# Optimization experiments

Measured on AMD Instinct MI355X. Metric: run time of the kernel, lower is better.

## Reference

```python
import jax, jax.numpy as jnp
import numpy as np


def setup_inputs() -> dict:
    key = jax.random.key(0)
    k1, k2 = jax.random.split(key)
    latents = jax.random.normal(k1, (32, 1024, 64), dtype=jnp.float32)
    codebook = jax.random.normal(k2, (8192, 64), dtype=jnp.float32)
    return {"latents": latents, "codebook": codebook}


def reference(latents, codebook):
    # Faithful to: cdist(latents_flat, codebook) -> argmin(dim=1) -> reshape(B, L)
    B, L, D = latents.shape
    x = latents.reshape(-1, D)                         # (N, D)
    x2 = jnp.sum(x * x, axis=1, keepdims=True)         # (N, 1)
    c2 = jnp.sum(codebook * codebook, axis=1)          # (K,)
    # (N, K) distance matrix, then argmin reduction
    d2 = x2 - 2.0 * (x @ codebook.T) + c2[None, :]
    indices = jnp.argmin(d2, axis=1)                   # (N,)
    return indices.reshape(B, L)
```

## Files before the change

kernel.cpp:

```cpp
#include <hip/hip_runtime.h>
#include <stdint.h>


#define N_TOTAL 32768
#define K_CODES 8192
#define EPS_GAP 0.008f

typedef __attribute__((ext_vector_type(4)))  float  floatx4;
typedef __attribute__((ext_vector_type(8)))  __bf16 bf16x8;

#define O_C2    0u
#define O_CBSW  32768u
#define O_PS1   2129920u
#define O_PS2   2654208u
#define O_PI1   3178496u
#define O_CNT   3702784u
#define O_LIST  3703040u
#define O_SLOT  3834112u
#define WS_NEED 4096256u

__device__ __forceinline__ unsigned int fkey(float s) {
    unsigned int u = __float_as_uint(s);
    return (u & 0x80000000u) ? ~u : (u | 0x80000000u);
}

__device__ __forceinline__ void load_lds16(const void* g, void* l) {
    __builtin_amdgcn_global_load_lds(
        (const __attribute__((address_space(1))) unsigned int*)g,
        (__attribute__((address_space(3))) unsigned int*)l, 16, 0, 0);
}

__global__ __launch_bounds__(256) void vq_prep(
    const float4* __restrict__ cb, uint4* __restrict__ cbSw,
    float* __restrict__ c2, int* __restrict__ cnt) {
    __shared__ float red[256];
    const int m = threadIdx.x & 31, g = threadIdx.x >> 5;
    const int rb = blockIdx.x;
    if (rb == 0 && threadIdx.x == 0) *cnt = 0;
    float4 a = cb[(size_t)(rb * 32 + m) * 16 + g * 2];
    float4 b = cb[(size_t)(rb * 32 + m) * 16 + g * 2 + 1];
    float x[8] = {a.x, a.y, a.z, a.w, b.x, b.y, b.z, b.w};
    bf16x8 hv, lv;
    float ss = 0.f;
#pragma unroll
    for (int i = 0; i < 8; ++i) {
        float v  = x[i];
        __bf16 hb = (__bf16)v;
        float r  = v - (float)hb;
        hv[i] = hb;
        lv[i] = (__bf16)r;
        ss += v * v;
    }
    cbSw[(size_t)rb * 512 + g * 32 + m]       = __builtin_bit_cast(uint4, hv);
    cbSw[(size_t)rb * 512 + (8 + g) * 32 + m] = __builtin_bit_cast(uint4, lv);
    red[threadIdx.x] = ss;
    __syncthreads();
    if (threadIdx.x < 32) {
        float s = 0.f;
#pragma unroll
        for (int gg = 0; gg < 8; ++gg) s += red[threadIdx.x + 32 * gg];
        c2[rb * 32 + threadIdx.x] = s;
    }
}

__global__ __launch_bounds__(256, 4) void vq_mfma(
    const float4* __restrict__ lat, const uint4* __restrict__ cbSw,
    const float* __restrict__ c2,
    float* __restrict__ pS1, float* __restrict__ pS2, int* __restrict__ pI1) {
    __shared__ uint4 Bs[2][1024];
    const int tid = threadIdx.x;
    const int wr = tid >> 6, lane = tid & 63;
    const int c16 = lane & 15, h4 = lane >> 4;

    const int q0 = blockIdx.x * 128 + wr * 32 + c16;
    bf16x8 aH[2][2], aL[2][2];
#pragma unroll
    for (int qt = 0; qt < 2; ++qt)
#pragma unroll
    for (int c = 0; c < 2; ++c) {
        float4 v0 = lat[(size_t)(q0 + qt * 16) * 16 + c * 8 + h4 * 2];
        float4 v1 = lat[(size_t)(q0 + qt * 16) * 16 + c * 8 + h4 * 2 + 1];
        float x[8] = {v0.x, v0.y, v0.z, v0.w, v1.x, v1.y, v1.z, v1.w};
#pragma unroll
        for (int j = 0; j < 8; ++j) {
            float v  = x[j];
            __bf16 hb = (__bf16)v;
            aH[qt][c][j] = hb;
            aL[qt][c][j] = (__bf16)(v - (float)hb);
        }
    }

    float t1[2][4], t2[2][4]; int i1[2][4];
#pragma unroll
    for (int qt = 0; qt < 2; ++qt)
#pragma unroll
    for (int r = 0; r < 4; ++r) { t1[qt][r] = -3e38f; t2[qt][r] = -3e38f; i1[qt][r] = 0; }

    const int kBase = blockIdx.y * 2048;
    const uint4* srcBase = cbSw + ((size_t)(kBase >> 5) << 9);
    const float* c2g = c2 + kBase + c16;

    float ccCur[4], ccNxt[4];
#pragma unroll
    for (int T = 0; T < 4; ++T) ccCur[T] = c2g[T * 16];
#pragma unroll
    for (int i = 0; i < 4; ++i)
        load_lds16(&srcBase[wr * 256 + i * 64 + lane], &Bs[0][wr * 256 + i * 64]);
    __syncthreads();

    int cur = 0;
    for (int stage = 0; stage < 32; ++stage) {
        if (stage + 1 < 32) {
            const uint4* sp = srcBase + (size_t)(stage + 1) * 1024;
#pragma unroll
            for (int i = 0; i < 4; ++i)
                load_lds16(&sp[wr * 256 + i * 64 + lane],
                           &Bs[cur ^ 1][wr * 256 + i * 64]);
#pragma unroll
            for (int T = 0; T < 4; ++T)
                ccNxt[T] = c2g[(stage + 1) * 64 + T * 16];
        }

        const int colBase = kBase + stage * 64 + c16;

        __builtin_amdgcn_s_setprio(1);
#pragma unroll
        for (int T = 0; T < 4; ++T) {
            const float nn = -0.5f * ccCur[T];
            const int col = colBase + T * 16;
            const int bb = (T >> 1) * 512 + (T & 1) * 16 + c16 + h4 * 32;
            bf16x8 bH0 = __builtin_bit_cast(bf16x8, Bs[cur][bb]);
            bf16x8 bH1 = __builtin_bit_cast(bf16x8, Bs[cur][bb + 128]);
            bf16x8 bL0 = __builtin_bit_cast(bf16x8, Bs[cur][bb + 256]);
            bf16x8 bL1 = __builtin_bit_cast(bf16x8, Bs[cur][bb + 384]);
#pragma unroll
            for (int qt = 0; qt < 2; ++qt) {
                floatx4 acc = {nn, nn, nn, nn};
                acc = __builtin_amdgcn_mfma_f32_16x16x32_bf16(aH[qt][0], bH0, acc, 0, 0, 0);
                acc = __builtin_amdgcn_mfma_f32_16x16x32_bf16(aH[qt][1], bH1, acc, 0, 0, 0);
                acc = __builtin_amdgcn_mfma_f32_16x16x32_bf16(aL[qt][0], bH0, acc, 0, 0, 0);
                acc = __builtin_amdgcn_mfma_f32_16x16x32_bf16(aL[qt][1], bH1, acc, 0, 0, 0);
                acc = __builtin_amdgcn_mfma_f32_16x16x32_bf16(aH[qt][0], bL0, acc, 0, 0, 0);
                acc = __builtin_amdgcn_mfma_f32_16x16x32_bf16(aH[qt][1], bL1, acc, 0, 0, 0);
#pragma unroll
                for (int r = 0; r < 4; ++r) {
                    float a = acc[r];
                    bool gt = a > t1[qt][r];
                    t2[qt][r] = __builtin_amdgcn_fmed3f(a, t1[qt][r], t2[qt][r]);
                    t1[qt][r] = fmaxf(t1[qt][r], a);
                    i1[qt][r] = gt ? col : i1[qt][r];
                }
            }
        }
        __builtin_amdgcn_s_setprio(0);

        __syncthreads();
#pragma unroll
        for (int T = 0; T < 4; ++T) ccCur[T] = ccNxt[T];
        cur ^= 1;
    }

#pragma unroll
    for (int mask = 1; mask <= 8; mask <<= 1) {
#pragma unroll
        for (int qt = 0; qt < 2; ++qt)
#pragma unroll
        for (int r = 0; r < 4; ++r) {
            float o1 = __shfl_xor(t1[qt][r], mask);
            float o2 = __shfl_xor(t2[qt][r], mask);
            int   oi = __shfl_xor(i1[qt][r], mask);
            float n2 = fmaxf(fmaxf(t2[qt][r], o2), fminf(t1[qt][r], o1));
            bool take = (o1 > t1[qt][r]) || (o1 == t1[qt][r] && oi < i1[qt][r]);
            t1[qt][r] = take ? o1 : t1[qt][r];
            i1[qt][r] = take ? oi : i1[qt][r];
            t2[qt][r] = n2;
        }
    }

    if (c16 == 0) {
        const int o0 = blockIdx.y * N_TOTAL;
#pragma unroll
        for (int qt = 0; qt < 2; ++qt) {
            const int qb = blockIdx.x * 128 + wr * 32 + qt * 16 + h4 * 4;
#pragma unroll
            for (int r = 0; r < 4; ++r) {
                pS1[o0 + qb + r] = -2.f * t1[qt][r];
                pS2[o0 + qb + r] = -2.f * t2[qt][r];
                pI1[o0 + qb + r] = i1[qt][r];
            }
        }
    }
}

__global__ void vq_merge4(const float* __restrict__ pS1, const float* __restrict__ pS2,
                          const int* __restrict__ pI1, int* __restrict__ out,
                          int* __restrict__ cnt, int* __restrict__ list,
                          unsigned long long* __restrict__ slot) {
    int q = blockIdx.x * 256 + threadIdx.x;
    float g1 = 3e38f, g2 = 3e38f;
    int   gi = 0x7FFFFFFF;
#pragma unroll
    for (int p = 0; p < 4; ++p) {
        float s1p = pS1[p * N_TOTAL + q];
        float s2p = pS2[p * N_TOTAL + q];
        int   i1p = pI1[p * N_TOTAL + q];
        bool take = (s1p < g1) || (s1p == g1 && i1p < gi);
        g2 = fminf(g2, fminf(s2p, take ? g1 : s1p));
        if (take) { g1 = s1p; gi = i1p; }
    }
    out[q] = gi;
    if (g2 - g1 < EPS_GAP) {
        int e = atomicAdd(cnt, 1);
        list[e] = q;
        slot[e] = 0xFFFFFFFFFFFFFFFFull;
    }
}

__global__ __launch_bounds__(256) void vq_exact2(
    const float4* __restrict__ lat, const float4* __restrict__ cb,
    const float* __restrict__ c2, const int* __restrict__ cnt,
    const int* __restrict__ list, unsigned long long* __restrict__ slot) {
    __shared__ float qv[4][64];
    const int n = *cnt;
    const int totalChunks = n * 8;
    const int wInB = threadIdx.x >> 6;
    const int lane = threadIdx.x & 63;

    for (int base = blockIdx.x * 4; base < totalChunks; base += gridDim.x * 4) {
        const int c = base + wInB;
        const bool act = c < totalChunks;
        int e = 0, q = 0, kb = 0;
        if (act) { e = c >> 3; q = list[e]; kb = (c & 7) << 10; }
        __syncthreads();
        if (act && lane < 16) {
            float4 v = lat[(size_t)q * 16 + lane];
            *(float4*)&qv[wInB][lane * 4] = v;
        }
        __syncthreads();
        if (act) {
            float best = 3e38f; int bi = 0;
#pragma unroll 2
            for (int i = 0; i < 16; ++i) {
                const int k = kb + i * 64 + lane;
                float dot = 0.f;
#pragma unroll
                for (int d4 = 0; d4 < 16; ++d4) {
                    float4 cv = cb[(size_t)k * 16 + d4];
                    dot += qv[wInB][d4 * 4 + 0] * cv.x + qv[wInB][d4 * 4 + 1] * cv.y
                         + qv[wInB][d4 * 4 + 2] * cv.z + qv[wInB][d4 * 4 + 3] * cv.w;
                }
                float s = c2[k] - 2.f * dot;
                if (s < best) { best = s; bi = k; }
            }
            unsigned long long p = ((unsigned long long)fkey(best) << 32) | (unsigned)bi;
#pragma unroll
            for (int mask = 1; mask <= 32; mask <<= 1) {
                unsigned long long o = __shfl_xor(p, mask);
                p = o < p ? o : p;
            }
            if (lane == 0) atomicMin(&slot[e], p);
        }
    }
}

__global__ void vq_write(const int* __restrict__ cnt, const int* __restrict__ list,
                         const unsigned long long* __restrict__ slot,
                         int* __restrict__ out) {
    int t = blockIdx.x * 256 + threadIdx.x;
    if (t < *cnt) out[list[t]] = (int)(slot[t] & 0xFFFFFFFFull);
}

#define BM 128
#define BN 128
#define PAD 68

__global__ void vq_norms_fb(const float4* __restrict__ cb, float* __restrict__ c2) {
    int t = blockIdx.x * 256 + threadIdx.x;
    int r = t >> 2, p = t & 3;
    float s = 0.f;
#pragma unroll
    for (int i = 0; i < 4; ++i) {
        float4 v = cb[r * 16 + p * 4 + i];
        s += v.x * v.x + v.y * v.y + v.z * v.z + v.w * v.w;
    }
    s += __shfl_xor(s, 1);
    s += __shfl_xor(s, 2);
    if (p == 0) c2[r] = s;
}

__global__ __launch_bounds__(256) void vq_fp32(
    const float4* __restrict__ lat, const float4* __restrict__ cb,
    const float* __restrict__ c2, int ktPer,
    int* __restrict__ outIdx, float* __restrict__ partS, int* __restrict__ partI,
    int writePartial) {
    __shared__ float As[BM][PAD];
    __shared__ float Bsf[BN][PAD];
    __shared__ float c2s[BN];
    const int tid = threadIdx.x;
    const int tx = tid & 15;
    const int ty = tid >> 4;
    const int nBase = blockIdx.x * BM;
    const int kt0 = blockIdx.y * ktPer;
    const int ktN = kt0 + ktPer;
#pragma unroll
    for (int r = 0; r < 8; ++r) {
        int f = tid + 256 * r;
        int mm = f >> 4, d4 = f & 15;
        float4 v = lat[(size_t)(nBase + mm) * 16 + d4];
        *(float4*)&As[mm][d4 * 4] = v;
    }
    float best[8]; int bidx[8];
#pragma unroll
    for (int ii = 0; ii < 8; ++ii) { best[ii] = 3e38f; bidx[ii] = 0; }
    for (int kt = kt0; kt < ktN; ++kt) {
        const int kbase = kt * BN;
        __syncthreads();
#pragma unroll
        for (int r = 0; r < 8; ++r) {
            int f = tid + 256 * r;
            int k = f >> 4, d4 = f & 15;
            float4 v = cb[(size_t)(kbase + k) * 16 + d4];
            *(float4*)&Bsf[k][d4 * 4] = v;
        }
        if (tid < BN) c2s[tid] = c2[kbase + tid];
        __syncthreads();
        float acc[8][8];
#pragma unroll
        for (int ii = 0; ii < 8; ++ii)
#pragma unroll
            for (int jj = 0; jj < 8; ++jj) acc[ii][jj] = 0.f;
#pragma unroll 4
        for (int d4 = 0; d4 < 16; ++d4) {
            float4 a[8], b[8];
#pragma unroll
            for (int ii = 0; ii < 8; ++ii) a[ii] = *(const float4*)&As[tx + 16 * ii][d4 * 4];
#pragma unroll
            for (int jj = 0; jj < 8; ++jj) b[jj] = *(const float4*)&Bsf[ty + 16 * jj][d4 * 4];
#pragma unroll
            for (int ii = 0; ii < 8; ++ii)
#pragma unroll
                for (int jj = 0; jj < 8; ++jj)
                    acc[ii][jj] += a[ii].x * b[jj].x + a[ii].y * b[jj].y
                                 + a[ii].z * b[jj].z + a[ii].w * b[jj].w;
        }
#pragma unroll
        for (int jj = 0; jj < 8; ++jj) {
            int k = kbase + ty + 16 * jj;
            float cc = c2s[ty + 16 * jj];
#pragma unroll
            for (int ii = 0; ii < 8; ++ii) {
                float s = cc - 2.f * acc[ii][jj];
                if (s < best[ii]) { best[ii] = s; bidx[ii] = k; }
            }
        }
    }
    __syncthreads();
    float* redS = &As[0][0];
    int*   redI = (int*)&Bsf[0][0];
#pragma unroll
    for (int ii = 0; ii < 8; ++ii) {
        int mm = tx + 16 * ii;
        redS[ty * BM + mm] = best[ii];
        redI[ty * BM + mm] = bidx[ii];
    }
    __syncthreads();
    if (tid < BM) {
        int mm = tid;
        float bs = redS[mm]; int bi = redI[mm];
#pragma unroll
        for (int t = 1; t < 16; ++t) {
            float s = redS[t * BM + mm]; int i = redI[t * BM + mm];
            if (s < bs || (s == bs && i < bi)) { bs = s; bi = i; }
        }
        int n = nBase + mm;
        if (writePartial) { partS[blockIdx.y * N_TOTAL + n] = bs; partI[blockIdx.y * N_TOTAL + n] = bi; }
        else outIdx[n] = bi;
    }
}

__global__ void vq_merge_fb(const float* __restrict__ partS, const int* __restrict__ partI,
                            int* __restrict__ out) {
    int n = blockIdx.x * 256 + threadIdx.x;
    float s0 = partS[n], s1 = partS[N_TOTAL + n];
    int   i0 = partI[n], i1 = partI[N_TOTAL + n];
    out[n] = (s1 < s0) ? i1 : i0;
}

extern "C" void kernel_launch(void* const* d_in, const int* in_sizes, int n_in,
                              void* d_out, int out_size, void* d_ws, size_t ws_size,
                              hipStream_t stream) {
    const float4* lat = (const float4*)d_in[0];
    const float4* cb  = (const float4*)d_in[1];
    int* out = (int*)d_out;
    char* ws = (char*)d_ws;

    if (ws_size >= WS_NEED) {
        float* c2   = (float*)(ws + O_C2);
        uint4* cbSw = (uint4*)(ws + O_CBSW);
        float* pS1  = (float*)(ws + O_PS1);
        float* pS2  = (float*)(ws + O_PS2);
        int*   pI1  = (int*)(ws + O_PI1);
        int*   cnt  = (int*)(ws + O_CNT);
        int*   list = (int*)(ws + O_LIST);
        unsigned long long* slot = (unsigned long long*)(ws + O_SLOT);

        vq_prep<<<256, 256, 0, stream>>>(cb, cbSw, c2, cnt);
        vq_mfma<<<dim3(256, 4), 256, 0, stream>>>(lat, cbSw, c2, pS1, pS2, pI1);
        vq_merge4<<<128, 256, 0, stream>>>(pS1, pS2, pI1, out, cnt, list, slot);
        vq_exact2<<<1024, 256, 0, stream>>>(lat, cb, c2, cnt, list, slot);
        vq_write<<<128, 256, 0, stream>>>(cnt, list, slot, out);
    } else {
        float* c2 = (float*)ws;
        vq_norms_fb<<<128, 256, 0, stream>>>(cb, c2);
        const size_t needSplit = 32768u + 2u * N_TOTAL * 4u + 2u * N_TOTAL * 4u + 64u;
        if (ws_size >= needSplit) {
            float* partS = (float*)(ws + 32768);
            int*   partI = (int*)(ws + 32768 + 2 * N_TOTAL * 4);
            dim3 grid(N_TOTAL / BM, 2);
            vq_fp32<<<grid, 256, 0, stream>>>(lat, cb, c2, (K_CODES / BN) / 2, out, partS, partI, 1);
            vq_merge_fb<<<N_TOTAL / 256, 256, 0, stream>>>(partS, partI, out);
        } else {
            dim3 grid(N_TOTAL / BM, 1);
            vq_fp32<<<grid, 256, 0, stream>>>(lat, cb, c2, K_CODES / BN, out, nullptr, nullptr, 0);
        }
    }
}
```

Before: 193.2 us.

## Use norm-scaled ambiguity threshold and rescan only ambiguous codebook quarters

The merge kernel now derives a per-query tolerance from the query norm and the maximum codebook norm, replacing the fixed gap constant. It also records which of the four codebook partitions have a runner-up within that tolerance, packed into the upper bits of the list entry. The exact fp32 rescoring pass then fully rescans only those flagged 2048-code partitions, and for the others re-scores just the partition's approximate winner. This cuts exact rescoring work, at the cost of an extra read of the latents and a codebook-norm max reduction in every merge block, and correctness now depends on the tolerance formula actually bounding the approximate-score error.

Result: slower. 210.4 us (+8.9%).

```diff
diff --git a/kernel.cpp b/kernel.cpp
--- a/kernel.cpp
+++ b/kernel.cpp
@@ -4,7 +4,6 @@
 
 #define N_TOTAL 32768
 #define K_CODES 8192
-#define EPS_GAP 0.008f
 
 typedef __attribute__((ext_vector_type(4)))  float  floatx4;
 typedef __attribute__((ext_vector_type(8)))  __bf16 bf16x8;
@@ -193,72 +192,115 @@
 }
 
 __global__ void vq_merge4(const float* __restrict__ pS1, const float* __restrict__ pS2,
-                          const int* __restrict__ pI1, int* __restrict__ out,
+                          const int* __restrict__ pI1, const float4* __restrict__ lat,
+                          const float* __restrict__ c2, int* __restrict__ out,
                           int* __restrict__ cnt, int* __restrict__ list,
                           unsigned long long* __restrict__ slot) {
-    int q = blockIdx.x * 256 + threadIdx.x;
+    __shared__ float bred[256];
+    float bm = 0.f;
+    for (int i = threadIdx.x; i < K_CODES; i += 256) bm = fmaxf(bm, c2[i]);
+    bred[threadIdx.x] = bm;
+    __syncthreads();
+    for (int s = 128; s > 0; s >>= 1) {
+        if (threadIdx.x < s)
+            bred[threadIdx.x] = fmaxf(bred[threadIdx.x], bred[threadIdx.x + s]);
+        __syncthreads();
+    }
+    const float Bmax = sqrtf(bred[0]);
+
+    const int q = blockIdx.x * 256 + threadIdx.x;
+    float x2 = 0.f;
+#pragma unroll
+    for (int d4 = 0; d4 < 16; ++d4) {
+        float4 v = lat[(size_t)q * 16 + d4];
+        x2 += v.x * v.x + v.y * v.y + v.z * v.z + v.w * v.w;
+    }
+    const float epsq = 4.58e-5f * sqrtf(x2) * Bmax + 1.2e-3f;
+
     float g1 = 3e38f, g2 = 3e38f;
     int   gi = 0x7FFFFFFF;
+    float s2v[4];
 #pragma unroll
     for (int p = 0; p < 4; ++p) {
         float s1p = pS1[p * N_TOTAL + q];
         float s2p = pS2[p * N_TOTAL + q];
         int   i1p = pI1[p * N_TOTAL + q];
+        s2v[p] = s2p;
         bool take = (s1p < g1) || (s1p == g1 && i1p < gi);
         g2 = fminf(g2, fminf(s2p, take ? g1 : s1p));
         if (take) { g1 = s1p; gi = i1p; }
     }
     out[q] = gi;
-    if (g2 - g1 < EPS_GAP) {
+    if (g2 - g1 < epsq) {
+        int msk = 0;
+#pragma unroll
+        for (int p = 0; p < 4; ++p)
+            if (s2v[p] - g1 < epsq) msk |= (1 << p);
         int e = atomicAdd(cnt, 1);
-        list[e] = q;
+        list[e] = q | (msk << 16);
         slot[e] = 0xFFFFFFFFFFFFFFFFull;
     }
 }
 
-__global__ __launch_bounds__(256) void vq_exact2(
-    const float4* __restrict__ lat, const float4* __restrict__ cb,
-    const float* __restrict__ c2, const int* __restrict__ cnt,
-    const int* __restrict__ list, unsigned long long* __restrict__ slot) {
+__global__ __launch_bounds__(256) void vq_exact3(
+    const float4* __restrict__ lat, const float* __restrict__ cbf,
+    const float* __restrict__ c2, const int* __restrict__ pI1,
+    const int* __restrict__ cnt, const int* __restrict__ list,
+    unsigned long long* __restrict__ slot) {
     __shared__ float qv[4][64];
     const int n = *cnt;
-    const int totalChunks = n * 8;
+    const int total = n * 4;
     const int wInB = threadIdx.x >> 6;
     const int lane = threadIdx.x & 63;
 
-    for (int base = blockIdx.x * 4; base < totalChunks; base += gridDim.x * 4) {
-        const int c = base + wInB;
-        const bool act = c < totalChunks;
-        int e = 0, q = 0, kb = 0;
-        if (act) { e = c >> 3; q = list[e]; kb = (c & 7) << 10; }
+    for (int base = blockIdx.x * 4; base < total; base += gridDim.x * 4) {
+        const int u = base + wInB;
+        const bool act = u < total;
+        int e = 0, p = 0, q = 0, msk = 0;
+        if (act) {
+            e = u >> 2; p = u & 3;
+            int v = list[e]; q = v & 0xFFFF; msk = v >> 16;
+        }
         __syncthreads();
         if (act && lane < 16) {
-            float4 v = lat[(size_t)q * 16 + lane];
-            *(float4*)&qv[wInB][lane * 4] = v;
+            float4 vv = lat[(size_t)q * 16 + lane];
+            *(float4*)&qv[wInB][lane * 4] = vv;
         }
         __syncthreads();
         if (act) {
-            float best = 3e38f; int bi = 0;
-#pragma unroll 2
-            for (int i = 0; i < 16; ++i) {
-                const int k = kb + i * 64 + lane;
-                float dot = 0.f;
-#pragma unroll
-                for (int d4 = 0; d4 < 16; ++d4) {
-                    float4 cv = cb[(size_t)k * 16 + d4];
-                    dot += qv[wInB][d4 * 4 + 0] * cv.x + qv[wInB][d4 * 4 + 1] * cv.y
-                         + qv[wInB][d4 * 4 + 2] * cv.z + qv[wInB][d4 * 4 + 3] * cv.w;
+            unsigned long long pk;
+            if ((msk >> p) & 1) {
+                float best = 3e38f; int bi = 0;
+                const int kb = p * 2048;
+                for (int i = 0; i < 32; ++i) {
+                    const int k = kb + i * 64 + lane;
+                    float dot = 0.f;
+                    const float4* cp = (const float4*)&cbf[(size_t)k * 64];
+#pragma unroll
+                    for (int d4 = 0; d4 < 16; ++d4) {
+                        float4 cv = cp[d4];
+                        dot += qv[wInB][d4 * 4 + 0] * cv.x + qv[wInB][d4 * 4 + 1] * cv.y
+                             + qv[wInB][d4 * 4 + 2] * cv.z + qv[wInB][d4 * 4 + 3] * cv.w;
+                    }
+                    float s = c2[k] - 2.f * dot;
+                    if (s < best) { best = s; bi = k; }
                 }
-                float s = c2[k] - 2.f * dot;
-                if (s < best) { best = s; bi = k; }
+                pk = ((unsigned long long)fkey(best) << 32) | (unsigned)bi;
+#pragma unroll
+                for (int mask = 1; mask <= 32; mask <<= 1) {
+                    unsigned long long o = __shfl_xor(pk, mask);
+                    pk = o < pk ? o : pk;
+                }
+            } else {
+                const int k = pI1[p * N_TOTAL + q];
+                float prod = qv[wInB][lane] * cbf[(size_t)k * 64 + lane];
+#pragma unroll
+                for (int mask = 1; mask <= 32; mask <<= 1)
+                    prod += __shfl_xor(prod, mask);
+                float s = c2[k] - 2.f * prod;
+                pk = ((unsigned long long)fkey(s) << 32) | (unsigned)k;
             }
-            unsigned long long p = ((unsigned long long)fkey(best) << 32) | (unsigned)bi;
-#pragma unroll
-            for (int mask = 1; mask <= 32; mask <<= 1) {
-                unsigned long long o = __shfl_xor(p, mask);
-                p = o < p ? o : p;
-            }
-            if (lane == 0) atomicMin(&slot[e], p);
+            if (lane == 0) atomicMin(&slot[e], pk);
         }
     }
 }
@@ -267,7 +309,7 @@
                          const unsigned long long* __restrict__ slot,
                          int* __restrict__ out) {
     int t = blockIdx.x * 256 + threadIdx.x;
-    if (t < *cnt) out[list[t]] = (int)(slot[t] & 0xFFFFFFFFull);
+    if (t < *cnt) out[list[t] & 0xFFFF] = (int)(slot[t] & 0xFFFFFFFFull);
 }
 
 #define BM 128
@@ -406,8 +448,8 @@
 
         vq_prep<<<256, 256, 0, stream>>>(cb, cbSw, c2, cnt);
         vq_mfma<<<dim3(256, 4), 256, 0, stream>>>(lat, cbSw, c2, pS1, pS2, pI1);
-        vq_merge4<<<128, 256, 0, stream>>>(pS1, pS2, pI1, out, cnt, list, slot);
-        vq_exact2<<<1024, 256, 0, stream>>>(lat, cb, c2, cnt, list, slot);
+        vq_merge4<<<128, 256, 0, stream>>>(pS1, pS2, pI1, lat, c2, out, cnt, list, slot);
+        vq_exact3<<<1024, 256, 0, stream>>>(lat, (const float*)cb, c2, pI1, cnt, list, slot);
         vq_write<<<128, 256, 0, stream>>>(cnt, list, slot, out);
     } else {
         float* c2 = (float*)ws;
```
